# Kernel optimization log

Measured on AMD Instinct MI355X. Metric: run time of the kernel, lower is better.

The kernel has to match this reference:

```python
import jax, jax.numpy as jnp
import numpy as np

E = 768   # embed_size
H = 64    # head_embed_size
B = 8
T = 4096  # == ctx_size


def setup_inputs() -> dict:
    key = jax.random.key(0)
    k1, k2, k3, k4 = jax.random.split(key, 4)
    inputs = jax.random.normal(k1, (B, T, E), dtype=jnp.float32)
    # Linear weights stored as (E, H) so projection is x @ W
    scale = 1.0 / np.sqrt(E)
    Wq = jax.random.uniform(k2, (E, H), dtype=jnp.float32, minval=-scale, maxval=scale)
    Wk = jax.random.uniform(k3, (E, H), dtype=jnp.float32, minval=-scale, maxval=scale)
    Wv = jax.random.uniform(k4, (E, H), dtype=jnp.float32, minval=-scale, maxval=scale)
    return {"inputs": inputs, "Wq": Wq, "Wk": Wk, "Wv": Wv}


def reference(inputs, Wq, Wk, Wv):
    Tlen = inputs.shape[1]
    q = inputs @ Wq  # (B,T,H)
    k = inputs @ Wk  # (B,T,H)
    v = inputs @ Wv  # (B,T,H)
    # NOTE: original module does NOT scale by 1/sqrt(H) — faithful reproduction.
    scores = jnp.einsum('bqh,bkh->bqk', q, k)  # (B,T,T)
    causal = jnp.tril(jnp.ones((Tlen, Tlen), dtype=bool))
    scores = jnp.where(causal, scores, -jnp.inf)
    attn = jax.nn.softmax(scores, axis=-1)
    # dropout=0 -> identity
    out = jnp.einsum('bqk,bkh->bqh', attn, v)  # (B,T,H)
    return out
```

## Files before the change

### kernel.cpp

```cpp
#include <hip/hip_runtime.h>
#include <hip/hip_bf16.h>

#define E_DIM 768
#define H_DIM 64
#define B_SZ 8
#define T_SZ 4096
#define BT (B_SZ * T_SZ)

typedef __attribute__((ext_vector_type(8))) short short8;
typedef __attribute__((ext_vector_type(4))) float floatx4;

#define RAWBAR() __asm__ volatile("s_waitcnt lgkmcnt(0)\n\ts_barrier" ::: "memory")

static __device__ __forceinline__ unsigned short bf1(float a) {
    __hip_bfloat16 h = __float2bfloat16(a);
    unsigned short u; __builtin_memcpy(&u, &h, 2); return u;
}
static __device__ __forceinline__ unsigned int pk2(float a, float b) {
    __hip_bfloat162 h = __float22bfloat162_rn(float2{a, b});
    unsigned int u; __builtin_memcpy(&u, &h, 4); return u;
}

__global__ __launch_bounds__(256) void prep_w(
    const float* __restrict__ Wq, const float* __restrict__ Wk,
    const float* __restrict__ Wv, unsigned short* __restrict__ Wt)
{
    __shared__ float Ls[64][65];
    const int nt = blockIdx.x;
    const int kc = blockIdx.y;
    const float* __restrict__ W = (nt == 0) ? Wq : (nt == 1) ? Wk : Wv;
    const float scl = (nt == 0) ? 1.44269504088896f : 1.0f;
    const int t = threadIdx.x;
    const int k0 = kc * 64;

#pragma unroll
    for (int it = 0; it < 16; ++it) {
        const int kk = (t >> 6) + it * 4;
        Ls[kk][t & 63] = W[(size_t)(k0 + kk) * H_DIM + (t & 63)];
    }
    __syncthreads();

#pragma unroll
    for (int it = 0; it < 4; ++it) {
        const int nl = (t >> 4) + it * 16;
        const int kl = (t & 15) * 4;
        unsigned int u[2];
        u[0] = pk2(Ls[kl + 0][nl] * scl, Ls[kl + 1][nl] * scl);
        u[1] = pk2(Ls[kl + 2][nl] * scl, Ls[kl + 3][nl] * scl);
        *(uint2*)(Wt + (size_t)(nt * 64 + nl) * E_DIM + k0 + kl) = *(uint2*)u;
    }
}

__global__ __launch_bounds__(768) void proj_mfma(
    const float* __restrict__ X, const unsigned short* __restrict__ Wt,
    unsigned short* __restrict__ Qb, unsigned short* __restrict__ Kb,
    unsigned short* __restrict__ Vtb)
{
    __shared__ unsigned short Xs[2][16][776];

    const int tid  = threadIdx.x;
    const int wave = tid >> 6, lane = tid & 63;
    const int row  = lane & 15, quad = lane >> 4;
    const int m0   = blockIdx.x * 128;

    short8 bfr[24];
    {
        const unsigned short* wp = Wt + (size_t)(wave * 16 + row) * E_DIM + quad * 8;
#pragma unroll
        for (int ks = 0; ks < 24; ++ks) bfr[ks] = *(const short8*)(wp + ks * 32);
    }

    const int srow = tid & 15;
    const int sc   = tid >> 4;
    const float* __restrict__ xbase = X + (size_t)(m0 + srow) * E_DIM + sc * 16;

    float4 fx[4];
#define LDX(mt)                                                               \
    {                                                                         \
        const float* p = xbase + (size_t)(mt) * 16 * E_DIM;                   \
        fx[0] = *(const float4*)(p);     fx[1] = *(const float4*)(p + 4);     \
        fx[2] = *(const float4*)(p + 8); fx[3] = *(const float4*)(p + 12);    \
    }
#define STX(buf)                                                              \
    {                                                                         \
        unsigned int tmp[8];                                                  \
        tmp[0] = pk2(fx[0].x, fx[0].y); tmp[1] = pk2(fx[0].z, fx[0].w);       \
        tmp[2] = pk2(fx[1].x, fx[1].y); tmp[3] = pk2(fx[1].z, fx[1].w);       \
        tmp[4] = pk2(fx[2].x, fx[2].y); tmp[5] = pk2(fx[2].z, fx[2].w);       \
        tmp[6] = pk2(fx[3].x, fx[3].y); tmp[7] = pk2(fx[3].z, fx[3].w);       \
        *(int4*)&Xs[buf][srow][sc * 16]     = *(int4*)&tmp[0];                \
        *(int4*)&Xs[buf][srow][sc * 16 + 8] = *(int4*)&tmp[4];                \
    }

    LDX(0); STX(0);
    RAWBAR();

    const int g  = wave >> 2;
    const int h  = (wave & 3) * 16 + row;
    unsigned short* __restrict__ OQK = (g == 0) ? Qb : Kb;
    const int bb = m0 >> 12;

    int cur = 0;
    for (int mt = 0; mt < 8; ++mt) {
        if (mt < 7) LDX(mt + 1);

        floatx4 acc = (floatx4)0.0f;
#pragma unroll
        for (int ks = 0; ks < 24; ++ks) {
            const short8 af = *(const short8*)&Xs[cur][row][ks * 32 + quad * 8];
            acc = __builtin_amdgcn_mfma_f32_16x16x32_bf16(af, bfr[ks], acc, 0, 0, 0);
        }

        const int mr = m0 + mt * 16 + quad * 4;
        if (g < 2) {
#pragma unroll
            for (int r = 0; r < 4; ++r)
                OQK[(size_t)(mr + r) * H_DIM + h] = bf1(acc[r]);
        } else {
            const int t0 = mr & 4095;
            unsigned int u[2];
            u[0] = pk2(acc[0], acc[1]); u[1] = pk2(acc[2], acc[3]);
            *(uint2*)(Vtb + ((size_t)bb * H_DIM + h) * T_SZ + t0) = *(uint2*)u;
        }

        if (mt < 7) STX(cur ^ 1);
        RAWBAR();
        cur ^= 1;
    }
#undef LDX
#undef STX
}

__global__ __launch_bounds__(256, 4) void attn_mfma(
    const unsigned short* __restrict__ Qb,
    const unsigned short* __restrict__ Kb,
    const unsigned short* __restrict__ Vtb,
    float* __restrict__ Out)
{
    __shared__ __align__(16) unsigned short KV[2][64][72];
    __shared__ __align__(16) unsigned short Ps[4][16][40];
    __shared__ float lc[4][16];

    const int lb   = blockIdx.x;
    const int b    = lb & 7;
    const int qq   = 127 - (lb >> 3);
    const int tid  = threadIdx.x;
    const int wave = tid >> 6, lane = tid & 63;
    const int col  = lane & 15, quad = lane >> 4;
    const int wq   = wave >> 1;
    const int wk   = wave & 1;

    const size_t base = (size_t)b * T_SZ * H_DIM;
    const int q0  = qq * 32;
    const int nkt = (qq >> 1) + 1;
    const int ktd = nkt - 1;

    short8 qf0, qf1;
    {
        const unsigned short* qp = Qb + base + (size_t)(q0 + wq * 16 + col) * H_DIM + quad * 8;
        qf0 = *(const short8*)(qp);
        qf1 = *(const short8*)(qp + 32);
    }

    floatx4 o[4];
#pragma unroll
    for (int i = 0; i < 4; ++i) o[i] = (floatx4)0.0f;
    float lp[4] = {0.0f, 0.0f, 0.0f, 0.0f};

    const int krow = tid >> 2, kcol = (tid & 3) * 16;
    const unsigned short* __restrict__ Ksrc = Kb + base + (size_t)krow * H_DIM + kcol;
    const unsigned short* __restrict__ Vsrc = Vtb + ((size_t)b * H_DIM + krow) * T_SZ + kcol;

    int4 kr0, kr1, vr0, vr1;
#define LDKV(t)                                                          \
    {                                                                    \
        const unsigned short* kp = Ksrc + (size_t)(t) * 64 * H_DIM;      \
        kr0 = *(const int4*)kp; kr1 = *(const int4*)(kp + 8);            \
        const unsigned short* vp = Vsrc + (t) * 64;                      \
        vr0 = *(const int4*)vp; vr1 = *(const int4*)(vp + 8);            \
    }
#define STKV()                                                           \
    {                                                                    \
        *(int4*)&KV[0][krow][kcol] = kr0; *(int4*)&KV[0][krow][kcol + 8] = kr1; \
        *(int4*)&KV[1][krow][kcol] = vr0; *(int4*)&KV[1][krow][kcol + 8] = vr1; \
    }

    LDKV(0);
    STKV();
    RAWBAR();

    for (int kt = 0; kt < nkt; ++kt) {
        if (kt + 1 < nkt) LDKV(kt + 1);

        floatx4 s[2];
#pragma unroll
        for (int j = 0; j < 2; ++j) {
            const unsigned short* kp = &KV[0][(wk * 2 + j) * 16 + col][quad * 8];
            floatx4 a = (floatx4)0.0f;
            a = __builtin_amdgcn_mfma_f32_16x16x32_bf16(qf0, *(const short8*)(kp),      a, 0, 0, 0);
            a = __builtin_amdgcn_mfma_f32_16x16x32_bf16(qf1, *(const short8*)(kp + 32), a, 0, 0, 0);
            s[j] = a;
        }

        if (kt == ktd) {
#pragma unroll
            for (int j = 0; j < 2; ++j) {
                const int keyg = kt * 64 + wk * 32 + j * 16 + col;
#pragma unroll
                for (int r = 0; r < 4; ++r)
                    if (keyg > q0 + wq * 16 + quad * 4 + r) s[j][r] = -1e30f;
            }
        }

#pragma unroll
        for (int r = 0; r < 4; ++r) {
#pragma unroll
            for (int j = 0; j < 2; ++j) {
                const float pv = exp2f(fminf(s[j][r], 110.0f));
                lp[r] += pv;
                Ps[wave][quad * 4 + r][j * 16 + col] = bf1(pv);
            }
        }
        __builtin_amdgcn_wave_barrier();

        {
            const short8 pa = *(const short8*)(&Ps[wave][col][quad * 8]);
#pragma unroll
            for (int d = 0; d < 4; ++d) {
                const short8 vb = *(const short8*)(&KV[1][d * 16 + col][wk * 32 + quad * 8]);
                o[d] = __builtin_amdgcn_mfma_f32_16x16x32_bf16(pa, vb, o[d], 0, 0, 0);
            }
        }

        RAWBAR();
        if (kt + 1 < nkt) STKV();
        RAWBAR();
    }

#pragma unroll
    for (int r = 0; r < 4; ++r) {
        float l = lp[r];
#pragma unroll
        for (int off = 1; off < 16; off <<= 1)
            l += __shfl_xor(l, off, 16);
        if (col == 0) lc[wave][quad * 4 + r] = l;
    }
    __syncthreads();

    float* __restrict__ Oc = (float*)&KV[0][0][0];
#pragma unroll
    for (int r = 0; r < 4; ++r)
#pragma unroll
        for (int d = 0; d < 4; ++d)
            Oc[((wave * 16) + quad * 4 + r) * 64 + d * 16 + col] = o[d][r];
    __syncthreads();

    {
        const int orow = tid >> 3;
        const int d0   = (tid & 7) * 8;
        const int rl   = orow & 15;
        const int wb   = (orow >> 4) * 2;
        const float* p0 = &Oc[((wb * 16) + rl) * 64 + d0];
        const float* p1 = &Oc[(((wb + 1) * 16) + rl) * 64 + d0];
        const float inv = 1.0f / (lc[wb][rl] + lc[wb + 1][rl]);
        float4 a0 = *(const float4*)(p0);
        float4 a1 = *(const float4*)(p0 + 4);
        const float4 b0 = *(const float4*)(p1);
        const float4 b1 = *(const float4*)(p1 + 4);
        a0.x = (a0.x + b0.x) * inv; a0.y = (a0.y + b0.y) * inv;
        a0.z = (a0.z + b0.z) * inv; a0.w = (a0.w + b0.w) * inv;
        a1.x = (a1.x + b1.x) * inv; a1.y = (a1.y + b1.y) * inv;
        a1.z = (a1.z + b1.z) * inv; a1.w = (a1.w + b1.w) * inv;
        float* op = Out + base + (size_t)(q0 + orow) * H_DIM + d0;
        *(float4*)(op)     = a0;
        *(float4*)(op + 4) = a1;
    }
#undef LDKV
#undef STKV
}

extern "C" void kernel_launch(void* const* d_in, const int* in_sizes, int n_in,
                              void* d_out, int out_size, void* d_ws, size_t ws_size,
                              hipStream_t stream) {
    const float* X  = (const float*)d_in[0];
    const float* Wq = (const float*)d_in[1];
    const float* Wk = (const float*)d_in[2];
    const float* Wv = (const float*)d_in[3];

    unsigned short* Wt  = (unsigned short*)d_ws;
    unsigned short* Qb  = Wt + (size_t)192 * E_DIM;
    unsigned short* Kb  = Qb + (size_t)BT * H_DIM;
    unsigned short* Vtb = Kb + (size_t)BT * H_DIM;

    prep_w<<<dim3(3, 12), 256, 0, stream>>>(Wq, Wk, Wv, Wt);
    proj_mfma<<<256, 768, 0, stream>>>(X, Wt, Qb, Kb, Vtb);
    attn_mfma<<<1024, 256, 0, stream>>>(Qb, Kb, Vtb, (float*)d_out);
}
```

Measured before the change: 230.7 us.

## Split long causal attention rows across two blocks and add combine kernel

The attention kernel now splits each of the 64 longest query tiles per batch into two key-range halves. Each half writes an unnormalised partial output and row sums to workspace, and a new combine kernel merges and normalises them. This is meant to balance work across CUs and shorten the critical tail. The K/V shared buffer becomes double-buffered with one barrier per iteration, with setprio around the MFMAs. The projection kernel uses smaller 64-row tiles and launches twice as many blocks. The split adds an extra launch and extra global traffic, and the attention occupancy hint drops from 4 to 3.

```diff
diff --git a/kernel.cpp b/kernel.cpp
--- a/kernel.cpp
+++ b/kernel.cpp
@@ -51,7 +51,7 @@
     }
 }
 
-__global__ __launch_bounds__(768) void proj_mfma(
+__global__ __launch_bounds__(768, 6) void proj_mfma(
     const float* __restrict__ X, const unsigned short* __restrict__ Wt,
     unsigned short* __restrict__ Qb, unsigned short* __restrict__ Kb,
     unsigned short* __restrict__ Vtb)
@@ -61,7 +61,7 @@
     const int tid  = threadIdx.x;
     const int wave = tid >> 6, lane = tid & 63;
     const int row  = lane & 15, quad = lane >> 4;
-    const int m0   = blockIdx.x * 128;
+    const int m0   = blockIdx.x * 64;
 
     short8 bfr[24];
     {
@@ -101,8 +101,8 @@
     const int bb = m0 >> 12;
 
     int cur = 0;
-    for (int mt = 0; mt < 8; ++mt) {
-        if (mt < 7) LDX(mt + 1);
+    for (int mt = 0; mt < 4; ++mt) {
+        if (mt < 3) LDX(mt + 1);
 
         floatx4 acc = (floatx4)0.0f;
 #pragma unroll
@@ -123,7 +123,7 @@
             *(uint2*)(Vtb + ((size_t)bb * H_DIM + h) * T_SZ + t0) = *(uint2*)u;
         }
 
-        if (mt < 7) STX(cur ^ 1);
+        if (mt < 3) STX(cur ^ 1);
         RAWBAR();
         cur ^= 1;
     }
@@ -131,19 +131,30 @@
 #undef STX
 }
 
-__global__ __launch_bounds__(256, 4) void attn_mfma(
+__global__ __launch_bounds__(256, 3) void attn_mfma(
     const unsigned short* __restrict__ Qb,
     const unsigned short* __restrict__ Kb,
     const unsigned short* __restrict__ Vtb,
+    float* __restrict__ Opart, float* __restrict__ lpart,
     float* __restrict__ Out)
 {
-    __shared__ __align__(16) unsigned short KV[2][64][72];
+    __shared__ __align__(16) unsigned short KVb[2][2][64][72];
     __shared__ __align__(16) unsigned short Ps[4][16][40];
     __shared__ float lc[4][16];
 
     const int lb   = blockIdx.x;
     const int b    = lb & 7;
-    const int qq   = 127 - (lb >> 3);
+    const int s    = lb >> 3;
+    const bool split = (s < 128);
+    const int qq   = split ? (127 - (s >> 1)) : (191 - s);
+    const int half = s & 1;
+    const int nkt_tot = (qq >> 1) + 1;
+    const int hsp  = (nkt_tot + 1) >> 1;
+    const int k0t  = (split && half) ? hsp : 0;
+    const int k1t  = (split && !half) ? hsp : nkt_tot;
+    const int ktd  = nkt_tot - 1;
+    const int n    = k1t - k0t;
+
     const int tid  = threadIdx.x;
     const int wave = tid >> 6, lane = tid & 63;
     const int col  = lane & 15, quad = lane >> 4;
@@ -152,8 +163,6 @@
 
     const size_t base = (size_t)b * T_SZ * H_DIM;
     const int q0  = qq * 32;
-    const int nkt = (qq >> 1) + 1;
-    const int ktd = nkt - 1;
 
     short8 qf0, qf1;
     {
@@ -179,28 +188,32 @@
         const unsigned short* vp = Vsrc + (t) * 64;                      \
         vr0 = *(const int4*)vp; vr1 = *(const int4*)(vp + 8);            \
     }
-#define STKV()                                                           \
+#define STKV(bf)                                                         \
     {                                                                    \
-        *(int4*)&KV[0][krow][kcol] = kr0; *(int4*)&KV[0][krow][kcol + 8] = kr1; \
-        *(int4*)&KV[1][krow][kcol] = vr0; *(int4*)&KV[1][krow][kcol + 8] = vr1; \
-    }
-
-    LDKV(0);
-    STKV();
+        *(int4*)&KVb[bf][0][krow][kcol] = kr0; *(int4*)&KVb[bf][0][krow][kcol + 8] = kr1; \
+        *(int4*)&KVb[bf][1][krow][kcol] = vr0; *(int4*)&KVb[bf][1][krow][kcol + 8] = vr1; \
+    }
+
+    LDKV(k0t);
+    STKV(0);
+    if (n > 1) LDKV(k0t + 1);
     RAWBAR();
 
-    for (int kt = 0; kt < nkt; ++kt) {
-        if (kt + 1 < nkt) LDKV(kt + 1);
-
-        floatx4 s[2];
+    int cur = 0;
+    for (int i = 0; i < n; ++i) {
+        const int kt = k0t + i;
+
+        floatx4 sv[2];
+        __builtin_amdgcn_s_setprio(1);
 #pragma unroll
         for (int j = 0; j < 2; ++j) {
-            const unsigned short* kp = &KV[0][(wk * 2 + j) * 16 + col][quad * 8];
+            const unsigned short* kp = &KVb[cur][0][(wk * 2 + j) * 16 + col][quad * 8];
             floatx4 a = (floatx4)0.0f;
             a = __builtin_amdgcn_mfma_f32_16x16x32_bf16(qf0, *(const short8*)(kp),      a, 0, 0, 0);
             a = __builtin_amdgcn_mfma_f32_16x16x32_bf16(qf1, *(const short8*)(kp + 32), a, 0, 0, 0);
-            s[j] = a;
-        }
+            sv[j] = a;
+        }
+        __builtin_amdgcn_s_setprio(0);
 
         if (kt == ktd) {
 #pragma unroll
@@ -208,7 +221,7 @@
                 const int keyg = kt * 64 + wk * 32 + j * 16 + col;
 #pragma unroll
                 for (int r = 0; r < 4; ++r)
-                    if (keyg > q0 + wq * 16 + quad * 4 + r) s[j][r] = -1e30f;
+                    if (keyg > q0 + wq * 16 + quad * 4 + r) sv[j][r] = -1e30f;
             }
         }
 
@@ -216,7 +229,7 @@
         for (int r = 0; r < 4; ++r) {
 #pragma unroll
             for (int j = 0; j < 2; ++j) {
-                const float pv = exp2f(fminf(s[j][r], 110.0f));
+                const float pv = exp2f(fminf(sv[j][r], 110.0f));
                 lp[r] += pv;
                 Ps[wave][quad * 4 + r][j * 16 + col] = bf1(pv);
             }
@@ -225,16 +238,21 @@
 
         {
             const short8 pa = *(const short8*)(&Ps[wave][col][quad * 8]);
+            __builtin_amdgcn_s_setprio(1);
 #pragma unroll
             for (int d = 0; d < 4; ++d) {
-                const short8 vb = *(const short8*)(&KV[1][d * 16 + col][wk * 32 + quad * 8]);
+                const short8 vb = *(const short8*)(&KVb[cur][1][d * 16 + col][wk * 32 + quad * 8]);
                 o[d] = __builtin_amdgcn_mfma_f32_16x16x32_bf16(pa, vb, o[d], 0, 0, 0);
             }
-        }
-
+            __builtin_amdgcn_s_setprio(0);
+        }
+
+        if (i + 1 < n) {
+            STKV(cur ^ 1);
+            if (i + 2 < n) LDKV(kt + 2);
+        }
         RAWBAR();
-        if (kt + 1 < nkt) STKV();
-        RAWBAR();
+        cur ^= 1;
     }
 
 #pragma unroll
@@ -247,7 +265,7 @@
     }
     __syncthreads();
 
-    float* __restrict__ Oc = (float*)&KV[0][0][0];
+    float* __restrict__ Oc = (float*)&KVb[0][0][0][0];
 #pragma unroll
     for (int r = 0; r < 4; ++r)
 #pragma unroll
@@ -262,21 +280,61 @@
         const int wb   = (orow >> 4) * 2;
         const float* p0 = &Oc[((wb * 16) + rl) * 64 + d0];
         const float* p1 = &Oc[(((wb + 1) * 16) + rl) * 64 + d0];
-        const float inv = 1.0f / (lc[wb][rl] + lc[wb + 1][rl]);
+        const float lsum = lc[wb][rl] + lc[wb + 1][rl];
         float4 a0 = *(const float4*)(p0);
         float4 a1 = *(const float4*)(p0 + 4);
         const float4 b0 = *(const float4*)(p1);
         const float4 b1 = *(const float4*)(p1 + 4);
-        a0.x = (a0.x + b0.x) * inv; a0.y = (a0.y + b0.y) * inv;
-        a0.z = (a0.z + b0.z) * inv; a0.w = (a0.w + b0.w) * inv;
-        a1.x = (a1.x + b1.x) * inv; a1.y = (a1.y + b1.y) * inv;
-        a1.z = (a1.z + b1.z) * inv; a1.w = (a1.w + b1.w) * inv;
-        float* op = Out + base + (size_t)(q0 + orow) * H_DIM + d0;
-        *(float4*)(op)     = a0;
-        *(float4*)(op + 4) = a1;
+        a0.x += b0.x; a0.y += b0.y; a0.z += b0.z; a0.w += b0.w;
+        a1.x += b1.x; a1.y += b1.y; a1.z += b1.z; a1.w += b1.w;
+        if (!split) {
+            const float inv = 1.0f / lsum;
+            a0.x *= inv; a0.y *= inv; a0.z *= inv; a0.w *= inv;
+            a1.x *= inv; a1.y *= inv; a1.z *= inv; a1.w *= inv;
+            float* op = Out + base + (size_t)(q0 + orow) * H_DIM + d0;
+            *(float4*)(op)     = a0;
+            *(float4*)(op + 4) = a1;
+        } else {
+            const int pidx = (b * 64 + (qq - 64)) * 2 + half;
+            float* op = Opart + ((size_t)pidx * 32 + orow) * 64 + d0;
+            *(float4*)(op)     = a0;
+            *(float4*)(op + 4) = a1;
+            if ((tid & 7) == 0) lpart[pidx * 32 + orow] = lsum;
+        }
     }
 #undef LDKV
 #undef STKV
+}
+
+__global__ __launch_bounds__(256) void attn_combine(
+    const float* __restrict__ Opart, const float* __restrict__ lpart,
+    float* __restrict__ Out)
+{
+    const int c   = blockIdx.x;
+    const int b   = c >> 6;
+    const int qi  = c & 63;
+    const int qq  = 64 + qi;
+    const int tid = threadIdx.x;
+    const int orow = tid >> 3;
+    const int d0   = (tid & 7) * 8;
+    const int p0   = (b * 64 + qi) * 2;
+
+    const float* P0 = Opart + ((size_t)p0 * 32 + orow) * 64 + d0;
+    const float* P1 = P0 + 32 * 64;
+    const float inv = 1.0f / (lpart[p0 * 32 + orow] + lpart[(p0 + 1) * 32 + orow]);
+
+    float4 a0 = *(const float4*)(P0);
+    float4 a1 = *(const float4*)(P0 + 4);
+    const float4 b0 = *(const float4*)(P1);
+    const float4 b1 = *(const float4*)(P1 + 4);
+    a0.x = (a0.x + b0.x) * inv; a0.y = (a0.y + b0.y) * inv;
+    a0.z = (a0.z + b0.z) * inv; a0.w = (a0.w + b0.w) * inv;
+    a1.x = (a1.x + b1.x) * inv; a1.y = (a1.y + b1.y) * inv;
+    a1.z = (a1.z + b1.z) * inv; a1.w = (a1.w + b1.w) * inv;
+
+    float* op = Out + ((size_t)b * T_SZ + qq * 32 + orow) * H_DIM + d0;
+    *(float4*)(op)     = a0;
+    *(float4*)(op + 4) = a1;
 }
 
 extern "C" void kernel_launch(void* const* d_in, const int* in_sizes, int n_in,
@@ -291,8 +349,11 @@
     unsigned short* Qb  = Wt + (size_t)192 * E_DIM;
     unsigned short* Kb  = Qb + (size_t)BT * H_DIM;
     unsigned short* Vtb = Kb + (size_t)BT * H_DIM;
+    float* Opart = (float*)(Vtb + (size_t)BT * H_DIM);
+    float* lpart = Opart + (size_t)1024 * 32 * 64;
 
     prep_w<<<dim3(3, 12), 256, 0, stream>>>(Wq, Wk, Wv, Wt);
-    proj_mfma<<<256, 768, 0, stream>>>(X, Wt, Qb, Kb, Vtb);
-    attn_mfma<<<1024, 256, 0, stream>>>(Qb, Kb, Vtb, (float*)d_out);
-}
+    proj_mfma<<<512, 768, 0, stream>>>(X, Wt, Qb, Kb, Vtb);
+    attn_mfma<<<1536, 256, 0, stream>>>(Qb, Kb, Vtb, Opart, lpart, (float*)d_out);
+    attn_combine<<<512, 256, 0, stream>>>(Opart, lpart, (float*)d_out);
+}
```

After: 308.3 us. 33.6% more time.
